# Kernel optimization log

Hardware: AMD Instinct MI355X
Metric: run time of the kernel (lower is better)

## Reference

```python
import jax, jax.numpy as jnp
import numpy as np

H, W = 2000, 1000  # T_out buffer: (1, 2000, 1000); conv spatial grid matches
FILL = -9999.0


def _winit(k, o, c):
    return jax.random.normal(k, (o, c), jnp.float32) * (1.0 / np.sqrt(c))


def setup_inputs() -> dict:
    key = jax.random.key(0)
    ks = jax.random.split(key, 6)
    inp = jax.random.normal(ks[0], (1, 9, H, W), dtype=jnp.float32)
    T_out = jnp.zeros((1, H, W), dtype=jnp.float32)
    flat = jnp.arange(H * W, dtype=jnp.int32)
    T_indices = jnp.stack([flat // W, flat % W]).reshape(2, H, W)
    return {
        "input": inp,
        "T_out": T_out,
        "T_indices": T_indices,
        "w1": _winit(ks[1], 18, 9), "b1": jnp.zeros((18,), jnp.float32),
        "w2": _winit(ks[2], 36, 18), "b2": jnp.zeros((36,), jnp.float32),
        "w3": _winit(ks[3], 36, 36), "b3": jnp.zeros((36,), jnp.float32),
        "w4": _winit(ks[4], 1, 36), "b4": jnp.zeros((1,), jnp.float32),
    }


def _conv1x1(x, w, b):
    # 1x1 conv == channel matmul: x (b,c,h,w), w (o,c)
    return jnp.einsum('bchw,oc->bohw', x, w) + b[None, :, None, None]


def reference(input, T_out, T_indices, w1, b1, w2, b2, w3, b3, w4, b4):
    x = jax.nn.relu(_conv1x1(input, w1, b1))
    x = jax.nn.relu(_conv1x1(x, w2, b2))
    x = jax.nn.relu(_conv1x1(x, w3, b3))
    x = _conv1x1(x, w4, b4)  # (1,1,H,W)
    # fill buffer with -9999 then indexed scatter of the fused scores
    T = jnp.full(T_out.shape, FILL, dtype=T_out.dtype)
    T = T.at[:, T_indices[0], T_indices[1]].set(x[0, 0])
    # MaxPool2d([1,1000]) -> max over W; MaxPool2d([2000,1]) -> max over H
    out1 = T.max(axis=2).squeeze()  # (2000,)
    out2 = T.max(axis=1).squeeze()  # (1000,)
    return (out1, out2)
```

## Files before the change

kernel.cpp:

```cpp
#include <hip/hip_runtime.h>

typedef _Float16 f16x8 __attribute__((ext_vector_type(8)));
typedef _Float16 f16x4 __attribute__((ext_vector_type(4)));
typedef __fp16 h16x2 __attribute__((ext_vector_type(2)));
typedef float f32x4 __attribute__((ext_vector_type(4)));

#define HH 2000
#define WW 1000
#define HWSZ (HH * WW)
#define NEG_INF (-3.0e38f)
#define RT 40

__device__ __forceinline__ unsigned fenc(float f) {
    unsigned u = __float_as_uint(f);
    return (u & 0x80000000u) ? ~u : (u | 0x80000000u);
}
__device__ __forceinline__ float fdec(unsigned k) {
    unsigned u = (k & 0x80000000u) ? (k & 0x7fffffffu) : ~k;
    return __uint_as_float(u);
}

__global__ void decode_buckets(unsigned* __restrict__ buck, int n) {
    int i = blockIdx.x * blockDim.x + threadIdx.x;
    if (i < n) {
        unsigned k = buck[i];
        ((float*)buck)[i] = fdec(k);
    }
}


__global__ __launch_bounds__(128) void mlp_max_mfma(
    const float* __restrict__ in,
    const float* __restrict__ w1, const float* __restrict__ b1,
    const float* __restrict__ w2, const float* __restrict__ b2,
    const float* __restrict__ w3, const float* __restrict__ b3,
    const float* __restrict__ w4, const float* __restrict__ b4,
    unsigned* __restrict__ rowbuck, unsigned* __restrict__ colbuck) {
    __shared__ _Float16 albuf[2][2 * 1280];
    __shared__ float rowsm[2][RT][16];

    const int tx = threadIdx.x;
    const int wv = threadIdx.y;
    const int px = tx & 15;
    const int q = tx >> 4;

    _Float16* s0buf1 = &albuf[wv][0];
    _Float16* s0buf2 = &albuf[wv][640];
    _Float16* s1buf1 = &albuf[wv][1280];
    _Float16* s1buf2 = &albuf[wv][1920];

    f16x8 A1[2], A2[3], A3s0[3], A3s1[3];
#pragma unroll
    for (int t = 0; t < 2; ++t) {
        const int m = t * 16 + px;
#pragma unroll
        for (int j = 0; j < 8; ++j) {
            const int k = q * 8 + j;
            float v = 0.f;
            if (m < 18) {
                if (k < 9) v = w1[m * 9 + k];
                else if (k == 9) v = b1[m];
            }
            A1[t][j] = (_Float16)v;
        }
    }
#pragma unroll
    for (int t = 0; t < 3; ++t) {
        const int m = t * 16 + px;
#pragma unroll
        for (int j = 0; j < 8; ++j) {
            const int k = q * 8 + j;
            float v = 0.f;
            if (m < 36) {
                if (k < 18) v = w2[m * 18 + k];
                else if (k == 18) v = b2[m];
            }
            A2[t][j] = (_Float16)v;
        }
    }
#pragma unroll
    for (int t = 0; t < 3; ++t) {
        const int m = t * 16 + px;
#pragma unroll
        for (int j = 0; j < 8; ++j) {
            const int k = q * 8 + j;
            float v = 0.f;
            if (m < 36 && k < 32) v = w3[m * 36 + k];
            A3s0[t][j] = (_Float16)v;
            float v2 = 0.f;
            const int k2 = 32 + k;
            if (m < 36) {
                if (k2 < 36) v2 = w3[m * 36 + k2];
                else if (k2 == 36) v2 = b3[m];
            }
            A3s1[t][j] = (_Float16)v2;
        }
    }

    float w4r[3][4];
#pragma unroll
    for (int t = 0; t < 3; ++t)
#pragma unroll
        for (int rg = 0; rg < 4; ++rg) {
            const int ch = t * 16 + q * 4 + rg;
            w4r[t][rg] = (ch < 36) ? w4[ch] : 0.f;
        }
    const float b4s = b4[0];

    const int col = blockIdx.x * 32 + wv * 16 + px;
    const int colc = (col < WW) ? col : (WW - 1);
    const bool colok = (col < WW);
    const int rb = blockIdx.y * RT;

    float colmax = NEG_INF;
    const f32x4 zf4 = {0.f, 0.f, 0.f, 0.f};
    const h16x2 z2 = {(__fp16)0.f, (__fp16)0.f};

    union U8 { f16x8 v; h16x2 h[4]; };
    union U4 { f16x4 v; h16x2 h[2]; };

    int off[8];
#pragma unroll
    for (int j = 0; j < 8; ++j) {
        const int c = q * 8 + j;
        off[j] = (c < 9) ? (c * HWSZ + colc) : 0;
    }

    float ca[8], cb[8], na[8], nb[8];

    auto LOAD = [&](int r, float (&v0)[8], float (&v1)[8]) {
        const float* rbase = in + (size_t)r * WW;
#pragma unroll
        for (int j = 0; j < 8; ++j) {
            const int c = q * 8 + j;
            float x0 = (c == 9) ? 1.f : 0.f;
            float x1 = x0;
            if (c < 9) {
                x0 = rbase[off[j]];
                x1 = rbase[off[j] + WW];
            }
            v0[j] = x0;
            v1[j] = x1;
        }
    };

    auto COMPUTE = [&](int it, const float (&v0)[8], const float (&v1)[8]) {
        U8 b0u, b1u;
#pragma unroll
        for (int j = 0; j < 4; ++j) {
            b0u.h[j] = __builtin_amdgcn_cvt_pkrtz(v0[2 * j], v0[2 * j + 1]);
            b1u.h[j] = __builtin_amdgcn_cvt_pkrtz(v1[2 * j], v1[2 * j + 1]);
        }
        const f16x8 bin0 = b0u.v;
        const f16x8 bin1 = b1u.v;

        f32x4 D1a[2], D1b[2];
#pragma unroll
        for (int t = 0; t < 2; ++t) {
            D1a[t] = __builtin_amdgcn_mfma_f32_16x16x32_f16(A1[t], bin0, zf4, 0, 0, 0);
            D1b[t] = __builtin_amdgcn_mfma_f32_16x16x32_f16(A1[t], bin1, zf4, 0, 0, 0);
        }
#pragma unroll
        for (int t = 0; t < 2; ++t) {
            U4 h0, h1;
            h0.h[0] = __builtin_elementwise_max(
                __builtin_amdgcn_cvt_pkrtz(D1a[t][0], D1a[t][1]), z2);
            h0.h[1] = __builtin_elementwise_max(
                __builtin_amdgcn_cvt_pkrtz(D1a[t][2], D1a[t][3]), z2);
            h1.h[0] = __builtin_elementwise_max(
                __builtin_amdgcn_cvt_pkrtz(D1b[t][0], D1b[t][1]), z2);
            h1.h[1] = __builtin_elementwise_max(
                __builtin_amdgcn_cvt_pkrtz(D1b[t][2], D1b[t][3]), z2);
            if (t == 1 && q == 0) {
                h0.v[2] = (_Float16)1.f;
                h1.v[2] = (_Float16)1.f;
            }
            *(f16x4*)&s0buf1[px * 40 + t * 16 + q * 4] = h0.v;
            *(f16x4*)&s1buf1[px * 40 + t * 16 + q * 4] = h1.v;
        }
        const f16x8 B2a = *(const f16x8*)&s0buf1[px * 40 + q * 8];
        const f16x8 B2b = *(const f16x8*)&s1buf1[px * 40 + q * 8];

        f32x4 D2a[3], D2b[3];
#pragma unroll
        for (int t = 0; t < 3; ++t) {
            D2a[t] = __builtin_amdgcn_mfma_f32_16x16x32_f16(A2[t], B2a, zf4, 0, 0, 0);
            D2b[t] = __builtin_amdgcn_mfma_f32_16x16x32_f16(A2[t], B2b, zf4, 0, 0, 0);
        }
#pragma unroll
        for (int t = 0; t < 3; ++t) {
            U4 h0, h1;
            h0.h[0] = __builtin_elementwise_max(
                __builtin_amdgcn_cvt_pkrtz(D2a[t][0], D2a[t][1]), z2);
            h0.h[1] = __builtin_elementwise_max(
                __builtin_amdgcn_cvt_pkrtz(D2a[t][2], D2a[t][3]), z2);
            h1.h[0] = __builtin_elementwise_max(
                __builtin_amdgcn_cvt_pkrtz(D2b[t][0], D2b[t][1]), z2);
            h1.h[1] = __builtin_elementwise_max(
                __builtin_amdgcn_cvt_pkrtz(D2b[t][2], D2b[t][3]), z2);
            if (t < 2) {
                *(f16x4*)&s0buf2[px * 40 + t * 16 + q * 4] = h0.v;
                *(f16x4*)&s1buf2[px * 40 + t * 16 + q * 4] = h1.v;
            } else if (q == 0) {
                *(f16x4*)&s0buf2[px * 40 + 32] = h0.v;
                *(f16x4*)&s1buf2[px * 40 + 32] = h1.v;
            }
        }
        const f16x8 B3a0 = *(const f16x8*)&s0buf2[px * 40 + q * 8];
        const f16x8 B3b0 = *(const f16x8*)&s1buf2[px * 40 + q * 8];
        f16x8 B3a1 = {0, 0, 0, 0, 0, 0, 0, 0};
        f16x8 B3b1 = {0, 0, 0, 0, 0, 0, 0, 0};
        if (q == 0) {
            const f16x4 t0 = *(const f16x4*)&s0buf2[px * 40 + 32];
            const f16x4 t1 = *(const f16x4*)&s1buf2[px * 40 + 32];
#pragma unroll
            for (int j = 0; j < 4; ++j) { B3a1[j] = t0[j]; B3b1[j] = t1[j]; }
            B3a1[4] = (_Float16)1.f;
            B3b1[4] = (_Float16)1.f;
        }

        f32x4 D3a[3], D3b[3];
#pragma unroll
        for (int t = 0; t < 3; ++t) {
            D3a[t] = __builtin_amdgcn_mfma_f32_16x16x32_f16(A3s0[t], B3a0, zf4, 0, 0, 0);
            D3a[t] = __builtin_amdgcn_mfma_f32_16x16x32_f16(A3s1[t], B3a1, D3a[t], 0, 0, 0);
            D3b[t] = __builtin_amdgcn_mfma_f32_16x16x32_f16(A3s0[t], B3b0, zf4, 0, 0, 0);
            D3b[t] = __builtin_amdgcn_mfma_f32_16x16x32_f16(A3s1[t], B3b1, D3b[t], 0, 0, 0);
        }

        float sa0 = 0.f, sa1 = 0.f, sa2 = 0.f, sa3 = 0.f;
        float sb0 = 0.f, sb1 = 0.f, sb2 = 0.f, sb3 = 0.f;
#pragma unroll
        for (int t = 0; t < 3; ++t) {
            sa0 = fmaf(w4r[t][0], fmaxf(D3a[t][0], 0.f), sa0);
            sa1 = fmaf(w4r[t][1], fmaxf(D3a[t][1], 0.f), sa1);
            sa2 = fmaf(w4r[t][2], fmaxf(D3a[t][2], 0.f), sa2);
            sa3 = fmaf(w4r[t][3], fmaxf(D3a[t][3], 0.f), sa3);
            sb0 = fmaf(w4r[t][0], fmaxf(D3b[t][0], 0.f), sb0);
            sb1 = fmaf(w4r[t][1], fmaxf(D3b[t][1], 0.f), sb1);
            sb2 = fmaf(w4r[t][2], fmaxf(D3b[t][2], 0.f), sb2);
            sb3 = fmaf(w4r[t][3], fmaxf(D3b[t][3], 0.f), sb3);
        }
        float sa = (sa0 + sa1) + (sa2 + sa3);
        float sb = (sb0 + sb1) + (sb2 + sb3);
        sa += __shfl_xor(sa, 16, 64); sb += __shfl_xor(sb, 16, 64);
        sa += __shfl_xor(sa, 32, 64); sb += __shfl_xor(sb, 32, 64);
        sa += b4s; sb += b4s;

        sa = colok ? sa : NEG_INF;
        sb = colok ? sb : NEG_INF;
        colmax = fmaxf(colmax, fmaxf(sa, sb));

        if (q == 0) rowsm[wv][it * 2][px] = sa;
        else if (q == 1) rowsm[wv][it * 2 + 1][px] = sb;
    };

    LOAD(rb, ca, cb);
#pragma unroll 1
    for (int it = 0; it < RT / 2; it += 2) {
        LOAD(rb + (it + 1) * 2, na, nb);
        COMPUTE(it, ca, cb);
        if (it < RT / 2 - 2) LOAD(rb + (it + 2) * 2, ca, cb);
        COMPUTE(it + 1, na, nb);
    }

    if (q == 0 && colok) atomicMax(&colbuck[col], fenc(colmax));
    if (tx < RT) {
        const f32x4 v0 = *(const f32x4*)&rowsm[wv][tx][0];
        const f32x4 v1 = *(const f32x4*)&rowsm[wv][tx][4];
        const f32x4 v2 = *(const f32x4*)&rowsm[wv][tx][8];
        const f32x4 v3 = *(const f32x4*)&rowsm[wv][tx][12];
        float m = NEG_INF;
#pragma unroll
        for (int j = 0; j < 4; ++j) {
            m = fmaxf(m, fmaxf(fmaxf(v0[j], v1[j]), fmaxf(v2[j], v3[j])));
        }
        atomicMax(&rowbuck[rb + tx], fenc(m));
    }
}

extern "C" void kernel_launch(void* const* d_in, const int* in_sizes, int n_in,
                              void* d_out, int out_size, void* d_ws, size_t ws_size,
                              hipStream_t stream) {
    const float* in = (const float*)d_in[0];
    const float* w1 = (const float*)d_in[3];
    const float* b1 = (const float*)d_in[4];
    const float* w2 = (const float*)d_in[5];
    const float* b2 = (const float*)d_in[6];
    const float* w3 = (const float*)d_in[7];
    const float* b3 = (const float*)d_in[8];
    const float* w4 = (const float*)d_in[9];
    const float* b4 = (const float*)d_in[10];

    unsigned* buck = (unsigned*)d_out;

    (void)hipMemsetAsync(buck, 0, 3000 * sizeof(unsigned), stream);

    dim3 block(64, 2);
    dim3 grid(32, 50);
    mlp_max_mfma<<<grid, block, 0, stream>>>(in, w1, b1, w2, b2, w3, b3, w4, b4,
                                             buck, buck + 2000);

    decode_buckets<<<(3000 + 255) / 256, 256, 0, stream>>>(buck, 3000);
}
```

Before: 190.7 us.

## Shrink row tile to 16 and move final reduction out of the per-step loop

Row tile per block drops from 40 to 16, so the grid grows from 32x50 to 32x125 blocks for more parallelism and better latency hiding. The per-step cross-lane shuffle reduction of the final dot product is replaced by writing partial sums to shared memory. The sums are then reduced once after the loop, which also computes the row and column maxima. The cost is more blocks, each paying a full weight-load prologue, and more column atomics.

After: 205.9 us. +7.9%, slower.

```diff
diff --git a/kernel.cpp b/kernel.cpp
--- a/kernel.cpp
+++ b/kernel.cpp
@@ -9,7 +9,6 @@
 #define WW 1000
 #define HWSZ (HH * WW)
 #define NEG_INF (-3.0e38f)
-#define RT 40
 
 __device__ __forceinline__ unsigned fenc(float f) {
     unsigned u = __float_as_uint(f);
@@ -37,7 +36,7 @@
     const float* __restrict__ w4, const float* __restrict__ b4,
     unsigned* __restrict__ rowbuck, unsigned* __restrict__ colbuck) {
     __shared__ _Float16 albuf[2][2 * 1280];
-    __shared__ float rowsm[2][RT][16];
+    __shared__ float psum[2][16][16][4];
 
     const int tx = threadIdx.x;
     const int wv = threadIdx.y;
@@ -107,12 +106,11 @@
         }
     const float b4s = b4[0];
 
-    const int col = blockIdx.x * 32 + wv * 16 + px;
+    const int col0 = blockIdx.x * 32 + wv * 16;
+    const int col = col0 + px;
     const int colc = (col < WW) ? col : (WW - 1);
-    const bool colok = (col < WW);
-    const int rb = blockIdx.y * RT;
-
-    float colmax = NEG_INF;
+    const int rb = blockIdx.y * 16;
+
     const f32x4 zf4 = {0.f, 0.f, 0.f, 0.f};
     const h16x2 z2 = {(__fp16)0.f, (__fp16)0.f};
 
@@ -241,41 +239,53 @@
             sb2 = fmaf(w4r[t][2], fmaxf(D3b[t][2], 0.f), sb2);
             sb3 = fmaf(w4r[t][3], fmaxf(D3b[t][3], 0.f), sb3);
         }
-        float sa = (sa0 + sa1) + (sa2 + sa3);
-        float sb = (sb0 + sb1) + (sb2 + sb3);
-        sa += __shfl_xor(sa, 16, 64); sb += __shfl_xor(sb, 16, 64);
-        sa += __shfl_xor(sa, 32, 64); sb += __shfl_xor(sb, 32, 64);
-        sa += b4s; sb += b4s;
-
-        sa = colok ? sa : NEG_INF;
-        sb = colok ? sb : NEG_INF;
-        colmax = fmaxf(colmax, fmaxf(sa, sb));
-
-        if (q == 0) rowsm[wv][it * 2][px] = sa;
-        else if (q == 1) rowsm[wv][it * 2 + 1][px] = sb;
+        const float sa = (sa0 + sa1) + (sa2 + sa3);
+        const float sb = (sb0 + sb1) + (sb2 + sb3);
+
+        psum[wv][it * 2][px][q] = sa;
+        psum[wv][it * 2 + 1][px][q] = sb;
     };
 
     LOAD(rb, ca, cb);
 #pragma unroll 1
-    for (int it = 0; it < RT / 2; it += 2) {
+    for (int it = 0; it < 8; it += 2) {
         LOAD(rb + (it + 1) * 2, na, nb);
         COMPUTE(it, ca, cb);
-        if (it < RT / 2 - 2) LOAD(rb + (it + 2) * 2, ca, cb);
+        if (it < 6) LOAD(rb + (it + 2) * 2, ca, cb);
         COMPUTE(it + 1, na, nb);
     }
 
-    if (q == 0 && colok) atomicMax(&colbuck[col], fenc(colmax));
-    if (tx < RT) {
-        const f32x4 v0 = *(const f32x4*)&rowsm[wv][tx][0];
-        const f32x4 v1 = *(const f32x4*)&rowsm[wv][tx][4];
-        const f32x4 v2 = *(const f32x4*)&rowsm[wv][tx][8];
-        const f32x4 v3 = *(const f32x4*)&rowsm[wv][tx][12];
-        float m = NEG_INF;
-#pragma unroll
-        for (int j = 0; j < 4; ++j) {
-            m = fmaxf(m, fmaxf(fmaxf(v0[j], v1[j]), fmaxf(v2[j], v3[j])));
-        }
-        atomicMax(&rowbuck[rb + tx], fenc(m));
+    {
+        const int row = tx >> 2;
+        const int pq = tx & 3;
+        float rmax = NEG_INF;
+        float cm[4];
+#pragma unroll
+        for (int g = 0; g < 4; ++g) {
+            const int p = pq * 4 + g;
+            const f32x4 v = *(const f32x4*)&psum[wv][row][p][0];
+            float s = (v[0] + v[1]) + (v[2] + v[3]) + b4s;
+            if (col0 + p >= WW) s = NEG_INF;
+            cm[g] = s;
+            rmax = fmaxf(rmax, s);
+        }
+        rmax = fmaxf(rmax, __shfl_xor(rmax, 1, 64));
+        rmax = fmaxf(rmax, __shfl_xor(rmax, 2, 64));
+        if (pq == 0) atomicMax(&rowbuck[rb + row], fenc(rmax));
+#pragma unroll
+        for (int g = 0; g < 4; ++g) {
+            cm[g] = fmaxf(cm[g], __shfl_xor(cm[g], 4, 64));
+            cm[g] = fmaxf(cm[g], __shfl_xor(cm[g], 8, 64));
+            cm[g] = fmaxf(cm[g], __shfl_xor(cm[g], 16, 64));
+            cm[g] = fmaxf(cm[g], __shfl_xor(cm[g], 32, 64));
+        }
+        if (row == 0) {
+#pragma unroll
+            for (int g = 0; g < 4; ++g) {
+                const int c = col0 + pq * 4 + g;
+                if (c < WW) atomicMax(&colbuck[c], fenc(cm[g]));
+            }
+        }
     }
 }
 
@@ -297,7 +307,7 @@
     (void)hipMemsetAsync(buck, 0, 3000 * sizeof(unsigned), stream);
 
     dim3 block(64, 2);
-    dim3 grid(32, 50);
+    dim3 grid(32, 125);
     mlp_max_mfma<<<grid, block, 0, stream>>>(in, w1, b1, w2, b2, w3, b3, w4, b4,
                                              buck, buck + 2000);
 
```
